# Performance work log

Hardware: AMD Instinct MI355X
Metric: run time of the kernel (lower is better)

## Reference

```python
import jax, jax.numpy as jnp
import numpy as np

HEAD_NUM = 8
QKV_DIM = 16
SQRT_EMBEDDING_DIM = 11.313708498984761  # sqrt(128)
LOGIT_CLIPPING = 10.0


def _reshape_by_heads(x):
    # x: [B, n, H*D] -> [B, H, n, D]
    B, n, _ = x.shape
    return x.reshape(B, n, HEAD_NUM, QKV_DIM).transpose(0, 2, 1, 3)


def setup_inputs() -> dict:
    key = jax.random.key(0)
    ks = jax.random.split(key, 12)
    B, P, N, E = 64, 500, 501, 128
    HD = HEAD_NUM * QKV_DIM
    s = 0.05
    return {
        "encoded_last_node": jax.random.normal(ks[0], (B, P, E), jnp.float32),
        "load": jax.random.uniform(ks[1], (B, P), jnp.float32),
        "ninf_mask": jnp.zeros((B, P, N), jnp.float32),
        "encoded_nodes": jax.random.normal(ks[2], (B, N, E), jnp.float32),
        "Wq_last": jax.random.normal(ks[3], (E + 1, HD), jnp.float32) * s,
        "Wk": jax.random.normal(ks[4], (E, HD), jnp.float32) * s,
        "Wv": jax.random.normal(ks[5], (E, HD), jnp.float32) * s,
        "mhc_W": jax.random.normal(ks[6], (HD, E), jnp.float32) * s,
        "mhc_b": jax.random.normal(ks[7], (E,), jnp.float32) * s,
        "new": jax.random.normal(ks[8], (B, HD, HD), jnp.float32) * s,
        "new_bias": jax.random.normal(ks[9], (B, 1, HD), jnp.float32) * s,
        "new_2": jax.random.normal(ks[10], (B, HD, HD), jnp.float32) * s,
        "new_bias_2": jax.random.normal(ks[11], (B, 1, HD), jnp.float32) * s,
    }


def reference(encoded_last_node, load, ninf_mask, encoded_nodes,
              Wq_last, Wk, Wv, mhc_W, mhc_b,
              new, new_bias, new_2, new_bias_2):
    B, P, E = encoded_last_node.shape
    # set_kv
    k = _reshape_by_heads(encoded_nodes @ Wk)            # [B,H,N,D]
    v = _reshape_by_heads(encoded_nodes @ Wv)            # [B,H,N,D]
    single_head_key = encoded_nodes.transpose(0, 2, 1)   # [B,E,N]

    # q from (last node embedding, load)
    input_cat = jnp.concatenate([encoded_last_node, load[:, :, None]], axis=2)  # [B,P,E+1]
    q = _reshape_by_heads(input_cat @ Wq_last)           # [B,H,P,D]

    # multi-head attention
    score = jnp.einsum('bhpd,bhnd->bhpn', q, k) / jnp.sqrt(jnp.float32(QKV_DIM))
    score = score + ninf_mask[:, None, :, :]
    attn = jax.nn.softmax(score, axis=3)
    out = jnp.einsum('bhpn,bhnd->bhpd', attn, v)         # [B,H,P,D]
    out_concat = out.transpose(0, 2, 1, 3).reshape(B, P, HEAD_NUM * QKV_DIM)

    # per-batch affine + relu + residual
    residual = out_concat
    h = jax.nn.relu(jnp.matmul(out_concat, new) + new_bias)
    h = jnp.matmul(h, new_2) + new_bias_2 + residual

    mh_atten_out = h @ mhc_W + mhc_b                     # [B,P,E]

    score2 = jnp.matmul(mh_atten_out, single_head_key)   # [B,P,N]
    score_clipped = LOGIT_CLIPPING * jnp.tanh(score2 / SQRT_EMBEDDING_DIM)
    probs = jax.nn.softmax(score_clipped + ninf_mask, axis=2)
    return probs
```

## Files before the change

kernel.cpp:

```cpp
#include <hip/hip_runtime.h>
#include <hip/hip_bf16.h>
#include <math.h>

typedef float f4 __attribute__((ext_vector_type(4)));

#define BATCH 64
#define PP 500
#define NN 501

__global__ __launch_bounds__(256) void k_proj_q(
    const float* __restrict__ Xn,
    const float* __restrict__ Ld,
    const float* __restrict__ Wq,
    float* __restrict__ Q)
{
  __shared__ float xs[64*132];
  const int t = threadIdx.x;
  const int r0 = blockIdx.x * 64;
  for (int i = t; i < 64*32; i += 256) {
    int r = i >> 5, k4 = (i & 31) << 2;
    *(f4*)(xs + r*132 + k4) = *(const f4*)(Xn + (size_t)(r0+r)*128 + k4);
  }
  if (t < 64) xs[t*132 + 128] = Ld[r0 + t];
  __syncthreads();
  const int tr = t >> 5, tc = t & 31;
  float acc[8][4];
  #pragma unroll
  for (int i = 0; i < 8; i++)
    #pragma unroll
    for (int c = 0; c < 4; c++) acc[i][c] = 0.f;
  for (int k4 = 0; k4 < 128; k4 += 4) {
    f4 x[8], w[4];
    #pragma unroll
    for (int j = 0; j < 4; j++) w[j] = *(const f4*)(Wq + (size_t)(k4+j)*128 + tc*4);
    #pragma unroll
    for (int i = 0; i < 8; i++) x[i] = *(const f4*)(xs + (tr*8+i)*132 + k4);
    #pragma unroll
    for (int i = 0; i < 8; i++)
      #pragma unroll
      for (int j = 0; j < 4; j++)
        #pragma unroll
        for (int c = 0; c < 4; c++)
          acc[i][c] += x[i][j] * w[j][c];
  }
  {
    f4 w = *(const f4*)(Wq + (size_t)128*128 + tc*4);
    #pragma unroll
    for (int i = 0; i < 8; i++) {
      float xv = xs[(tr*8+i)*132 + 128];
      #pragma unroll
      for (int c = 0; c < 4; c++) acc[i][c] += xv * w[c];
    }
  }
  #pragma unroll
  for (int i = 0; i < 8; i++) {
    f4 o;
    #pragma unroll
    for (int c = 0; c < 4; c++) o[c] = acc[i][c];
    *(f4*)(Q + (size_t)(r0 + tr*8 + i)*128 + tc*4) = o;
  }
}

__global__ __launch_bounds__(256) void k_proj_kv(
    const float* __restrict__ Xn,
    const float* __restrict__ Wk, const float* __restrict__ Wv,
    float* __restrict__ K_, float* __restrict__ V_)
{
  __shared__ float xs[64*132];
  const int t = threadIdx.x;
  const int r0 = blockIdx.x * 64;
  for (int i = t; i < 64*32; i += 256) {
    int r = i >> 5, k4 = (i & 31) << 2;
    *(f4*)(xs + r*132 + k4) = *(const f4*)(Xn + (size_t)(r0+r)*128 + k4);
  }
  __syncthreads();
  const int tr = t >> 5, tc = t & 31;
  float accK[8][4], accV[8][4];
  #pragma unroll
  for (int i = 0; i < 8; i++)
    #pragma unroll
    for (int c = 0; c < 4; c++) { accK[i][c] = 0.f; accV[i][c] = 0.f; }
  for (int k4 = 0; k4 < 128; k4 += 4) {
    f4 x[8], wk[4], wv[4];
    #pragma unroll
    for (int j = 0; j < 4; j++) {
      wk[j] = *(const f4*)(Wk + (size_t)(k4+j)*128 + tc*4);
      wv[j] = *(const f4*)(Wv + (size_t)(k4+j)*128 + tc*4);
    }
    #pragma unroll
    for (int i = 0; i < 8; i++) x[i] = *(const f4*)(xs + (tr*8+i)*132 + k4);
    #pragma unroll
    for (int i = 0; i < 8; i++)
      #pragma unroll
      for (int j = 0; j < 4; j++)
        #pragma unroll
        for (int c = 0; c < 4; c++) {
          accK[i][c] += x[i][j] * wk[j][c];
          accV[i][c] += x[i][j] * wv[j][c];
        }
  }
  #pragma unroll
  for (int i = 0; i < 8; i++) {
    f4 ok, ov;
    #pragma unroll
    for (int c = 0; c < 4; c++) { ok[c] = accK[i][c]; ov[c] = accV[i][c]; }
    *(f4*)(K_ + (size_t)(r0 + tr*8 + i)*128 + tc*4) = ok;
    *(f4*)(V_ + (size_t)(r0 + tr*8 + i)*128 + tc*4) = ov;
  }
}

__global__ __launch_bounds__(256, 3) void k_attn(
    const float* __restrict__ Q, const float* __restrict__ K_, const float* __restrict__ V_,
    const float* __restrict__ Msk, float* __restrict__ OC)
{
  __shared__ float ks[32*132];
  __shared__ float vs[32*132];
  __shared__ float mks[32*33];
  const int blk = blockIdx.x;
  const int b  = blk >> 4;
  const int pt = blk & 15;
  const int p0 = pt * 32;
  const int t = threadIdx.x;
  const int h   = t >> 5;
  const int row = t & 31;
  const bool pvalid = (p0 + row) < PP;
  const int p = pvalid ? (p0 + row) : (PP - 1);

  f4 q0, q1, q2, q3;
  {
    const float* qrow = Q + ((size_t)b*PP + p)*128 + h*16;
    q0 = *(const f4*)(qrow);
    q1 = *(const f4*)(qrow + 4);
    q2 = *(const f4*)(qrow + 8);
    q3 = *(const f4*)(qrow + 12);
  }
  const float* mgrow = Msk + ((size_t)b*PP + p)*NN;

  float m_r = -1e30f, l_r = 0.f;
  f4 o0 = {0.f,0.f,0.f,0.f}, o1 = o0, o2 = o0, o3 = o0;

  for (int c0 = 0; c0 < NN; c0 += 32) {
    __syncthreads();
    #pragma unroll
    for (int u = 0; u < 4; u++) {
      int i = t + u*256;
      int n = i >> 5, d4 = (i & 31) << 2;
      int ng = c0 + n;
      f4 kv = {0.f,0.f,0.f,0.f}, vv = {0.f,0.f,0.f,0.f};
      if (ng < NN) {
        kv = *(const f4*)(K_ + ((size_t)b*NN + ng)*128 + d4);
        vv = *(const f4*)(V_ + ((size_t)b*NN + ng)*128 + d4);
      }
      *(f4*)(ks + n*132 + d4) = kv;
      *(f4*)(vs + n*132 + d4) = vv;
    }
    {
      int mr = t >> 3, nq = (t & 7) << 2;
      int grow = p0 + mr; if (grow >= PP) grow = PP - 1;
      const float* gm = Msk + ((size_t)b*PP + grow)*NN + c0;
      float* dm = mks + mr*33 + nq;
      #pragma unroll
      for (int j = 0; j < 4; j++)
        dm[j] = (c0 + nq + j < NN) ? gm[nq + j] : -1e30f;
    }
    __syncthreads();

    const float* ksh = ks + h*16;
    const float* vsh = vs + h*16;
    const float* mrw = mks + row*33;
    #pragma unroll
    for (int n = 0; n < 32; n++) {
      const float* kf = ksh + n*132;
      f4 k0 = *(const f4*)(kf);
      f4 k1 = *(const f4*)(kf + 4);
      f4 k2 = *(const f4*)(kf + 8);
      f4 k3 = *(const f4*)(kf + 12);
      float s = 0.f;
      #pragma unroll
      for (int d = 0; d < 4; d++) s += q0[d]*k0[d];
      #pragma unroll
      for (int d = 0; d < 4; d++) s += q1[d]*k1[d];
      #pragma unroll
      for (int d = 0; d < 4; d++) s += q2[d]*k2[d];
      #pragma unroll
      for (int d = 0; d < 4; d++) s += q3[d]*k3[d];
      s = s*0.25f + mrw[n];
      if (s > m_r) {
        float cc = __expf(m_r - s);
        m_r = s;
        l_r *= cc;
        o0 *= cc; o1 *= cc; o2 *= cc; o3 *= cc;
      }
      float e = __expf(s - m_r);
      l_r += e;
      const float* vf = vsh + n*132;
      o0 += e * *(const f4*)(vf);
      o1 += e * *(const f4*)(vf + 4);
      o2 += e * *(const f4*)(vf + 8);
      o3 += e * *(const f4*)(vf + 12);
    }
  }

  if (pvalid) {
    float inv = 1.f / l_r;
    float* orow = OC + ((size_t)b*PP + p)*128 + h*16;
    *(f4*)(orow)      = o0 * inv;
    *(f4*)(orow + 4)  = o1 * inv;
    *(f4*)(orow + 8)  = o2 * inv;
    *(f4*)(orow + 12) = o3 * inv;
  }
}

__global__ __launch_bounds__(256) void k_ffn(
    const float* __restrict__ OC, const float* __restrict__ Wn, const float* __restrict__ Bn,
    const float* __restrict__ Wn2, const float* __restrict__ Bn2,
    const float* __restrict__ Wm, const float* __restrict__ Bm,
    float* __restrict__ MH)
{
  __shared__ float xs[64*132];
  __shared__ float hs[64*132];
  const int blk = blockIdx.x; const int b = blk >> 3, rb = blk & 7;
  const int r0 = rb*64;
  const int nv = min(64, PP - r0);
  const int t = threadIdx.x;
  const int tr = t >> 5, tc = t & 31;
  const float* ocb = OC + (size_t)b*PP*128;
  for (int i = t; i < 64*32; i += 256) {
    int r = i >> 5, k4 = (i & 31) << 2;
    f4 v = {0.f,0.f,0.f,0.f};
    if (r < nv) v = *(const f4*)(ocb + (size_t)(r0+r)*128 + k4);
    *(f4*)(xs + r*132 + k4) = v;
  }
  __syncthreads();
  {
    const float* W1 = Wn + (size_t)b*16384;
    float acc[8][4];
    #pragma unroll
    for (int i = 0; i < 8; i++)
      #pragma unroll
      for (int c = 0; c < 4; c++) acc[i][c] = 0.f;
    for (int k4 = 0; k4 < 128; k4 += 4) {
      f4 x[8], w[4];
      #pragma unroll
      for (int j = 0; j < 4; j++) w[j] = *(const f4*)(W1 + (size_t)(k4+j)*128 + tc*4);
      #pragma unroll
      for (int i = 0; i < 8; i++) x[i] = *(const f4*)(xs + (tr*8+i)*132 + k4);
      #pragma unroll
      for (int i = 0; i < 8; i++)
        #pragma unroll
        for (int j = 0; j < 4; j++)
          #pragma unroll
          for (int c = 0; c < 4; c++)
            acc[i][c] += x[i][j] * w[j][c];
    }
    f4 b1 = *(const f4*)(Bn + b*128 + tc*4);
    #pragma unroll
    for (int i = 0; i < 8; i++) {
      f4 o;
      #pragma unroll
      for (int c = 0; c < 4; c++) o[c] = fmaxf(acc[i][c] + b1[c], 0.f);
      *(f4*)(hs + (tr*8+i)*132 + tc*4) = o;
    }
  }
  __syncthreads();
  float h2[8][4];
  {
    const float* W2 = Wn2 + (size_t)b*16384;
    float acc[8][4];
    #pragma unroll
    for (int i = 0; i < 8; i++)
      #pragma unroll
      for (int c = 0; c < 4; c++) acc[i][c] = 0.f;
    for (int k4 = 0; k4 < 128; k4 += 4) {
      f4 x[8], w[4];
      #pragma unroll
      for (int j = 0; j < 4; j++) w[j] = *(const f4*)(W2 + (size_t)(k4+j)*128 + tc*4);
      #pragma unroll
      for (int i = 0; i < 8; i++) x[i] = *(const f4*)(hs + (tr*8+i)*132 + k4);
      #pragma unroll
      for (int i = 0; i < 8; i++)
        #pragma unroll
        for (int j = 0; j < 4; j++)
          #pragma unroll
          for (int c = 0; c < 4; c++)
            acc[i][c] += x[i][j] * w[j][c];
    }
    f4 b2 = *(const f4*)(Bn2 + b*128 + tc*4);
    #pragma unroll
    for (int i = 0; i < 8; i++)
      #pragma unroll
      for (int c = 0; c < 4; c++)
        h2[i][c] = acc[i][c] + b2[c] + xs[(tr*8+i)*132 + tc*4 + c];
  }
  __syncthreads();
  #pragma unroll
  for (int i = 0; i < 8; i++) {
    f4 o;
    #pragma unroll
    for (int c = 0; c < 4; c++) o[c] = h2[i][c];
    *(f4*)(hs + (tr*8+i)*132 + tc*4) = o;
  }
  __syncthreads();
  {
    float acc[8][4];
    #pragma unroll
    for (int i = 0; i < 8; i++)
      #pragma unroll
      for (int c = 0; c < 4; c++) acc[i][c] = 0.f;
    for (int k4 = 0; k4 < 128; k4 += 4) {
      f4 x[8], w[4];
      #pragma unroll
      for (int j = 0; j < 4; j++) w[j] = *(const f4*)(Wm + (size_t)(k4+j)*128 + tc*4);
      #pragma unroll
      for (int i = 0; i < 8; i++) x[i] = *(const f4*)(hs + (tr*8+i)*132 + k4);
      #pragma unroll
      for (int i = 0; i < 8; i++)
        #pragma unroll
        for (int j = 0; j < 4; j++)
          #pragma unroll
          for (int c = 0; c < 4; c++)
            acc[i][c] += x[i][j] * w[j][c];
    }
    f4 b3 = *(const f4*)(Bm + tc*4);
    #pragma unroll
    for (int i = 0; i < 8; i++) {
      if (tr*8 + i < nv) {
        f4 o;
        #pragma unroll
        for (int c = 0; c < 4; c++) o[c] = acc[i][c] + b3[c];
        *(f4*)(MH + ((size_t)b*PP + r0 + tr*8 + i)*128 + tc*4) = o;
      }
    }
  }
}

__global__ __launch_bounds__(256, 3) void k_final(
    const float* __restrict__ MH, const float* __restrict__ EN,
    const float* __restrict__ Msk, float* __restrict__ OUT)
{
  __shared__ float ms[32*132];
  __shared__ float es[64*132];
  const int blk = blockIdx.x; const int b = blk >> 4, rb = blk & 15;
  const int r0 = rb*32; const int nv = min(32, PP - r0);
  const int t = threadIdx.x;
  const int tr = t >> 5, tc = t & 31;
  const float* mhb = MH + (size_t)(b*PP + r0)*128;
  for (int i = t; i < 32*32; i += 256) {
    int r = i >> 5, k4 = (i & 31) << 2;
    f4 v = {0.f,0.f,0.f,0.f};
    if (r < nv) v = *(const f4*)(mhb + (size_t)r*128 + k4);
    *(f4*)(ms + r*132 + k4) = v;
  }
  const float* enb = EN + (size_t)b*NN*128;
  float s[8][4][2];
  #pragma unroll
  for (int nt = 0; nt < 8; nt++) {
    const int n0 = nt*64;
    __syncthreads();
    for (int i = t; i < 64*32; i += 256) {
      int n = i >> 5, k4 = (i & 31) << 2;
      f4 v = {0.f,0.f,0.f,0.f};
      if (n0 + n < NN) v = *(const f4*)(enb + (size_t)(n0+n)*128 + k4);
      *(f4*)(es + n*132 + k4) = v;
    }
    __syncthreads();
    float acc[4][2];
    #pragma unroll
    for (int i = 0; i < 4; i++) { acc[i][0] = 0.f; acc[i][1] = 0.f; }
    #pragma unroll 8
    for (int k4 = 0; k4 < 128; k4 += 4) {
      f4 x[4];
      #pragma unroll
      for (int i = 0; i < 4; i++) x[i] = *(const f4*)(ms + (tr*4+i)*132 + k4);
      f4 e0 = *(const f4*)(es + tc*132 + k4);
      f4 e1 = *(const f4*)(es + (tc+32)*132 + k4);
      #pragma unroll
      for (int i = 0; i < 4; i++)
        #pragma unroll
        for (int j = 0; j < 4; j++) {
          acc[i][0] += x[i][j]*e0[j];
          acc[i][1] += x[i][j]*e1[j];
        }
    }
    #pragma unroll
    for (int i = 0; i < 4; i++) {
      s[nt][i][0] = acc[i][0];
      s[nt][i][1] = acc[i][1];
    }
  }
  const float* mkb = Msk + (size_t)(b*PP + r0)*NN;
  #pragma unroll
  for (int nt = 0; nt < 8; nt++)
    #pragma unroll
    for (int i = 0; i < 4; i++)
      #pragma unroll
      for (int c = 0; c < 2; c++) {
        int r = tr*4 + i, n = nt*64 + tc + c*32;
        float val = -INFINITY;
        if (r < nv && n < NN) {
          float E = __expf(s[nt][i][c] * 0.17677669529663687f);
          val = 10.f - 20.f/(E + 1.f) + mkb[(size_t)r*NN + n];
        }
        s[nt][i][c] = val;
      }
  float* ob = OUT + (size_t)(b*PP + r0)*NN;
  #pragma unroll
  for (int i = 0; i < 4; i++) {
    float m = -INFINITY;
    #pragma unroll
    for (int nt = 0; nt < 8; nt++)
      #pragma unroll
      for (int c = 0; c < 2; c++) m = fmaxf(m, s[nt][i][c]);
    #pragma unroll
    for (int o = 16; o > 0; o >>= 1) m = fmaxf(m, __shfl_xor(m, o, 32));
    float l = 0.f;
    #pragma unroll
    for (int nt = 0; nt < 8; nt++)
      #pragma unroll
      for (int c = 0; c < 2; c++) {
        float e_ = __expf(s[nt][i][c] - m);
        s[nt][i][c] = e_;
        l += e_;
      }
    #pragma unroll
    for (int o = 16; o > 0; o >>= 1) l += __shfl_xor(l, o, 32);
    const int r = tr*4 + i;
    if (r < nv) {
      float inv = 1.f / l;
      float* orow = ob + (size_t)r*NN;
      #pragma unroll
      for (int nt = 0; nt < 8; nt++)
        #pragma unroll
        for (int c = 0; c < 2; c++) {
          int n = nt*64 + tc + c*32;
          if (n < NN) orow[n] = s[nt][i][c] * inv;
        }
    }
  }
}

extern "C" void kernel_launch(void* const* d_in, const int* in_sizes, int n_in,
                              void* d_out, int out_size, void* d_ws, size_t ws_size,
                              hipStream_t stream) {
  const float* eln  = (const float*)d_in[0];
  const float* load = (const float*)d_in[1];
  const float* mask = (const float*)d_in[2];
  const float* en   = (const float*)d_in[3];
  const float* Wq   = (const float*)d_in[4];
  const float* Wk   = (const float*)d_in[5];
  const float* Wv   = (const float*)d_in[6];
  const float* Wm   = (const float*)d_in[7];
  const float* Bm   = (const float*)d_in[8];
  const float* Wn   = (const float*)d_in[9];
  const float* Bn   = (const float*)d_in[10];
  const float* Wn2  = (const float*)d_in[11];
  const float* Bn2  = (const float*)d_in[12];
  float* out = (float*)d_out;
  float* ws  = (float*)d_ws;
  float* Q   = ws;
  float* K_  = ws + 4096000;
  float* V_  = ws + 8200192;
  float* OC  = ws + 12304384;
  float* MH  = ws + 16400384;
  hipLaunchKernelGGL(k_proj_q,  dim3(500),  dim3(256), 0, stream, eln, load, Wq, Q);
  hipLaunchKernelGGL(k_proj_kv, dim3(501),  dim3(256), 0, stream, en, Wk, Wv, K_, V_);
  hipLaunchKernelGGL(k_attn,    dim3(1024), dim3(256), 0, stream, Q, K_, V_, mask, OC);
  hipLaunchKernelGGL(k_ffn,     dim3(512),  dim3(256), 0, stream, OC, Wn, Bn, Wn2, Bn2, Wm, Bm, MH);
  hipLaunchKernelGGL(k_final,   dim3(1024), dim3(256), 0, stream, MH, en, mask, out);
}
```

Baseline: 443.5 us.

## Merge Q/KV projections into one launch and double attention rows per thread

```diff
diff --git a/kernel.cpp b/kernel.cpp
--- a/kernel.cpp
+++ b/kernel.cpp
@@ -8,104 +8,99 @@
 #define PP 500
 #define NN 501
 
-__global__ __launch_bounds__(256) void k_proj_q(
+__global__ __launch_bounds__(256) void k_proj(
+    const float* __restrict__ Xq,
+    const float* __restrict__ Ld,
     const float* __restrict__ Xn,
-    const float* __restrict__ Ld,
     const float* __restrict__ Wq,
-    float* __restrict__ Q)
+    const float* __restrict__ Wk, const float* __restrict__ Wv,
+    float* __restrict__ Q, float* __restrict__ K_, float* __restrict__ V_)
 {
   __shared__ float xs[64*132];
   const int t = threadIdx.x;
-  const int r0 = blockIdx.x * 64;
-  for (int i = t; i < 64*32; i += 256) {
-    int r = i >> 5, k4 = (i & 31) << 2;
-    *(f4*)(xs + r*132 + k4) = *(const f4*)(Xn + (size_t)(r0+r)*128 + k4);
-  }
-  if (t < 64) xs[t*132 + 128] = Ld[r0 + t];
-  __syncthreads();
   const int tr = t >> 5, tc = t & 31;
-  float acc[8][4];
-  #pragma unroll
-  for (int i = 0; i < 8; i++)
-    #pragma unroll
-    for (int c = 0; c < 4; c++) acc[i][c] = 0.f;
-  for (int k4 = 0; k4 < 128; k4 += 4) {
-    f4 x[8], w[4];
-    #pragma unroll
-    for (int j = 0; j < 4; j++) w[j] = *(const f4*)(Wq + (size_t)(k4+j)*128 + tc*4);
-    #pragma unroll
-    for (int i = 0; i < 8; i++) x[i] = *(const f4*)(xs + (tr*8+i)*132 + k4);
-    #pragma unroll
-    for (int i = 0; i < 8; i++)
-      #pragma unroll
-      for (int j = 0; j < 4; j++)
-        #pragma unroll
-        for (int c = 0; c < 4; c++)
-          acc[i][c] += x[i][j] * w[j][c];
-  }
-  {
-    f4 w = *(const f4*)(Wq + (size_t)128*128 + tc*4);
+  if (blockIdx.x < 500) {
+    const int r0 = blockIdx.x * 64;
+    for (int i = t; i < 64*32; i += 256) {
+      int r = i >> 5, k4 = (i & 31) << 2;
+      *(f4*)(xs + r*132 + k4) = *(const f4*)(Xq + (size_t)(r0+r)*128 + k4);
+    }
+    if (t < 64) xs[t*132 + 128] = Ld[r0 + t];
+    __syncthreads();
+    float acc[8][4];
+    #pragma unroll
+    for (int i = 0; i < 8; i++)
+      #pragma unroll
+      for (int c = 0; c < 4; c++) acc[i][c] = 0.f;
+    for (int k4 = 0; k4 < 128; k4 += 4) {
+      f4 x[8], w[4];
+      #pragma unroll
+      for (int j = 0; j < 4; j++) w[j] = *(const f4*)(Wq + (size_t)(k4+j)*128 + tc*4);
+      #pragma unroll
+      for (int i = 0; i < 8; i++) x[i] = *(const f4*)(xs + (tr*8+i)*132 + k4);
+      #pragma unroll
+      for (int i = 0; i < 8; i++)
+        #pragma unroll
+        for (int j = 0; j < 4; j++)
+          #pragma unroll
+          for (int c = 0; c < 4; c++)
+            acc[i][c] += x[i][j] * w[j][c];
+    }
+    {
+      f4 w = *(const f4*)(Wq + (size_t)128*128 + tc*4);
+      #pragma unroll
+      for (int i = 0; i < 8; i++) {
+        float xv = xs[(tr*8+i)*132 + 128];
+        #pragma unroll
+        for (int c = 0; c < 4; c++) acc[i][c] += xv * w[c];
+      }
+    }
     #pragma unroll
     for (int i = 0; i < 8; i++) {
-      float xv = xs[(tr*8+i)*132 + 128];
-      #pragma unroll
-      for (int c = 0; c < 4; c++) acc[i][c] += xv * w[c];
-    }
-  }
-  #pragma unroll
-  for (int i = 0; i < 8; i++) {
-    f4 o;
-    #pragma unroll
-    for (int c = 0; c < 4; c++) o[c] = acc[i][c];
-    *(f4*)(Q + (size_t)(r0 + tr*8 + i)*128 + tc*4) = o;
-  }
-}
-
-__global__ __launch_bounds__(256) void k_proj_kv(
-    const float* __restrict__ Xn,
-    const float* __restrict__ Wk, const float* __restrict__ Wv,
-    float* __restrict__ K_, float* __restrict__ V_)
-{
-  __shared__ float xs[64*132];
-  const int t = threadIdx.x;
-  const int r0 = blockIdx.x * 64;
-  for (int i = t; i < 64*32; i += 256) {
-    int r = i >> 5, k4 = (i & 31) << 2;
-    *(f4*)(xs + r*132 + k4) = *(const f4*)(Xn + (size_t)(r0+r)*128 + k4);
-  }
-  __syncthreads();
-  const int tr = t >> 5, tc = t & 31;
-  float accK[8][4], accV[8][4];
-  #pragma unroll
-  for (int i = 0; i < 8; i++)
-    #pragma unroll
-    for (int c = 0; c < 4; c++) { accK[i][c] = 0.f; accV[i][c] = 0.f; }
-  for (int k4 = 0; k4 < 128; k4 += 4) {
-    f4 x[8], wk[4], wv[4];
-    #pragma unroll
-    for (int j = 0; j < 4; j++) {
-      wk[j] = *(const f4*)(Wk + (size_t)(k4+j)*128 + tc*4);
-      wv[j] = *(const f4*)(Wv + (size_t)(k4+j)*128 + tc*4);
-    }
-    #pragma unroll
-    for (int i = 0; i < 8; i++) x[i] = *(const f4*)(xs + (tr*8+i)*132 + k4);
-    #pragma unroll
-    for (int i = 0; i < 8; i++)
-      #pragma unroll
-      for (int j = 0; j < 4; j++)
-        #pragma unroll
-        for (int c = 0; c < 4; c++) {
-          accK[i][c] += x[i][j] * wk[j][c];
-          accV[i][c] += x[i][j] * wv[j][c];
-        }
-  }
-  #pragma unroll
-  for (int i = 0; i < 8; i++) {
-    f4 ok, ov;
-    #pragma unroll
-    for (int c = 0; c < 4; c++) { ok[c] = accK[i][c]; ov[c] = accV[i][c]; }
-    *(f4*)(K_ + (size_t)(r0 + tr*8 + i)*128 + tc*4) = ok;
-    *(f4*)(V_ + (size_t)(r0 + tr*8 + i)*128 + tc*4) = ov;
+      f4 o;
+      #pragma unroll
+      for (int c = 0; c < 4; c++) o[c] = acc[i][c];
+      *(f4*)(Q + (size_t)(r0 + tr*8 + i)*128 + tc*4) = o;
+    }
+  } else {
+    const int r0 = (blockIdx.x - 500) * 64;
+    for (int i = t; i < 64*32; i += 256) {
+      int r = i >> 5, k4 = (i & 31) << 2;
+      *(f4*)(xs + r*132 + k4) = *(const f4*)(Xn + (size_t)(r0+r)*128 + k4);
+    }
+    __syncthreads();
+    float accK[8][4], accV[8][4];
+    #pragma unroll
+    for (int i = 0; i < 8; i++)
+      #pragma unroll
+      for (int c = 0; c < 4; c++) { accK[i][c] = 0.f; accV[i][c] = 0.f; }
+    for (int k4 = 0; k4 < 128; k4 += 4) {
+      f4 x[8], wk[4], wv[4];
+      #pragma unroll
+      for (int j = 0; j < 4; j++) {
+        wk[j] = *(const f4*)(Wk + (size_t)(k4+j)*128 + tc*4);
+        wv[j] = *(const f4*)(Wv + (size_t)(k4+j)*128 + tc*4);
+      }
+      #pragma unroll
+      for (int i = 0; i < 8; i++) x[i] = *(const f4*)(xs + (tr*8+i)*132 + k4);
+      #pragma unroll
+      for (int i = 0; i < 8; i++)
+        #pragma unroll
+        for (int j = 0; j < 4; j++)
+          #pragma unroll
+          for (int c = 0; c < 4; c++) {
+            accK[i][c] += x[i][j] * wk[j][c];
+            accV[i][c] += x[i][j] * wv[j][c];
+          }
+    }
+    #pragma unroll
+    for (int i = 0; i < 8; i++) {
+      f4 ok, ov;
+      #pragma unroll
+      for (int c = 0; c < 4; c++) { ok[c] = accK[i][c]; ov[c] = accV[i][c]; }
+      *(f4*)(K_ + (size_t)(r0 + tr*8 + i)*128 + tc*4) = ok;
+      *(f4*)(V_ + (size_t)(r0 + tr*8 + i)*128 + tc*4) = ov;
+    }
   }
 }
 
@@ -113,31 +108,38 @@
     const float* __restrict__ Q, const float* __restrict__ K_, const float* __restrict__ V_,
     const float* __restrict__ Msk, float* __restrict__ OC)
 {
-  __shared__ float ks[32*132];
-  __shared__ float vs[32*132];
-  __shared__ float mks[32*33];
+  __shared__ float ks[32*128];
+  __shared__ float vs[32*128];
+  __shared__ float mkt[32*64];
   const int blk = blockIdx.x;
-  const int b  = blk >> 4;
-  const int pt = blk & 15;
-  const int p0 = pt * 32;
+  const int b  = blk >> 3;
+  const int pt = blk & 7;
+  const int p0 = pt * 64;
   const int t = threadIdx.x;
-  const int h   = t >> 5;
-  const int row = t & 31;
-  const bool pvalid = (p0 + row) < PP;
-  const int p = pvalid ? (p0 + row) : (PP - 1);
-
-  f4 q0, q1, q2, q3;
+  const int h    = t >> 5;
+  const int rowA = t & 31;
+  const int rowB = rowA + 32;
+  const int pA = p0 + rowA;
+  const int pB0 = p0 + rowB;
+  const bool bvalid = pB0 < PP;
+  const int pB = bvalid ? pB0 : (PP - 1);
+
+  f4 qA0, qA1, qA2, qA3, qB0, qB1, qB2, qB3;
   {
-    const float* qrow = Q + ((size_t)b*PP + p)*128 + h*16;
-    q0 = *(const f4*)(qrow);
-    q1 = *(const f4*)(qrow + 4);
-    q2 = *(const f4*)(qrow + 8);
-    q3 = *(const f4*)(qrow + 12);
-  }
-  const float* mgrow = Msk + ((size_t)b*PP + p)*NN;
-
-  float m_r = -1e30f, l_r = 0.f;
-  f4 o0 = {0.f,0.f,0.f,0.f}, o1 = o0, o2 = o0, o3 = o0;
+    const float* qa = Q + ((size_t)b*PP + pA)*128 + h*16;
+    qA0 = *(const f4*)(qa); qA1 = *(const f4*)(qa+4); qA2 = *(const f4*)(qa+8); qA3 = *(const f4*)(qa+12);
+    const float* qb = Q + ((size_t)b*PP + pB)*128 + h*16;
+    qB0 = *(const f4*)(qb); qB1 = *(const f4*)(qb+4); qB2 = *(const f4*)(qb+8); qB3 = *(const f4*)(qb+12);
+  }
+
+  float mA = -1e30f, lA = 0.f, mB = -1e30f, lB = 0.f;
+  f4 oA0 = {0.f,0.f,0.f,0.f}, oA1 = oA0, oA2 = oA0, oA3 = oA0;
+  f4 oB0 = oA0, oB1 = oA0, oB2 = oA0, oB3 = oA0;
+
+  const int mr = t >> 3;
+  const int nq = (t & 7) << 2;
+  const float* gmA = Msk + ((size_t)b*PP + p0 + mr)*NN;
+  const float* gmB = Msk + ((size_t)b*PP + min(p0 + mr + 32, PP-1))*NN;
 
   for (int c0 = 0; c0 < NN; c0 += 32) {
     __syncthreads();
@@ -151,63 +153,72 @@
         kv = *(const f4*)(K_ + ((size_t)b*NN + ng)*128 + d4);
         vv = *(const f4*)(V_ + ((size_t)b*NN + ng)*128 + d4);
       }
-      *(f4*)(ks + n*132 + d4) = kv;
-      *(f4*)(vs + n*132 + d4) = vv;
-    }
-    {
-      int mr = t >> 3, nq = (t & 7) << 2;
-      int grow = p0 + mr; if (grow >= PP) grow = PP - 1;
-      const float* gm = Msk + ((size_t)b*PP + grow)*NN + c0;
-      float* dm = mks + mr*33 + nq;
-      #pragma unroll
-      for (int j = 0; j < 4; j++)
-        dm[j] = (c0 + nq + j < NN) ? gm[nq + j] : -1e30f;
-    }
-    __syncthreads();
-
-    const float* ksh = ks + h*16;
-    const float* vsh = vs + h*16;
-    const float* mrw = mks + row*33;
+      *(f4*)(ks + n*128 + d4) = kv;
+      *(f4*)(vs + n*128 + d4) = vv;
+    }
+    #pragma unroll
+    for (int j = 0; j < 4; j++) {
+      int nn = c0 + nq + j;
+      bool cv = nn < NN;
+      float a  = cv ? gmA[nn] : -1e30f;
+      float bb = cv ? gmB[nn] : -1e30f;
+      mkt[(nq+j)*64 + mr]      = a;
+      mkt[(nq+j)*64 + mr + 32] = bb;
+    }
+    __syncthreads();
+
     #pragma unroll
     for (int n = 0; n < 32; n++) {
-      const float* kf = ksh + n*132;
+      const float* kf = ks + n*128 + h*16;
       f4 k0 = *(const f4*)(kf);
       f4 k1 = *(const f4*)(kf + 4);
       f4 k2 = *(const f4*)(kf + 8);
       f4 k3 = *(const f4*)(kf + 12);
-      float s = 0.f;
-      #pragma unroll
-      for (int d = 0; d < 4; d++) s += q0[d]*k0[d];
-      #pragma unroll
-      for (int d = 0; d < 4; d++) s += q1[d]*k1[d];
-      #pragma unroll
-      for (int d = 0; d < 4; d++) s += q2[d]*k2[d];
-      #pragma unroll
-      for (int d = 0; d < 4; d++) s += q3[d]*k3[d];
-      s = s*0.25f + mrw[n];
-      if (s > m_r) {
-        float cc = __expf(m_r - s);
-        m_r = s;
-        l_r *= cc;
-        o0 *= cc; o1 *= cc; o2 *= cc; o3 *= cc;
-      }
-      float e = __expf(s - m_r);
-      l_r += e;
-      const float* vf = vsh + n*132;
-      o0 += e * *(const f4*)(vf);
-      o1 += e * *(const f4*)(vf + 4);
-      o2 += e * *(const f4*)(vf + 8);
-      o3 += e * *(const f4*)(vf + 12);
-    }
-  }
-
-  if (pvalid) {
-    float inv = 1.f / l_r;
-    float* orow = OC + ((size_t)b*PP + p)*128 + h*16;
-    *(f4*)(orow)      = o0 * inv;
-    *(f4*)(orow + 4)  = o1 * inv;
-    *(f4*)(orow + 8)  = o2 * inv;
-    *(f4*)(orow + 12) = o3 * inv;
+      float sA = 0.f, sB = 0.f;
+      #pragma unroll
+      for (int d = 0; d < 4; d++) {
+        sA += qA0[d]*k0[d]; sB += qB0[d]*k0[d];
+        sA += qA1[d]*k1[d]; sB += qB1[d]*k1[d];
+        sA += qA2[d]*k2[d]; sB += qB2[d]*k2[d];
+        sA += qA3[d]*k3[d]; sB += qB3[d]*k3[d];
+      }
+      sA = sA*0.25f + mkt[n*64 + rowA];
+      sB = sB*0.25f + mkt[n*64 + rowB];
+      if (sA > mA) {
+        float cc = __expf(mA - sA); mA = sA; lA *= cc;
+        oA0 *= cc; oA1 *= cc; oA2 *= cc; oA3 *= cc;
+      }
+      if (sB > mB) {
+        float cc = __expf(mB - sB); mB = sB; lB *= cc;
+        oB0 *= cc; oB1 *= cc; oB2 *= cc; oB3 *= cc;
+      }
+      float eA = __expf(sA - mA); lA += eA;
+      float eB = __expf(sB - mB); lB += eB;
+      const float* vf = vs + n*128 + h*16;
+      f4 v0 = *(const f4*)(vf);
+      f4 v1 = *(const f4*)(vf + 4);
+      f4 v2 = *(const f4*)(vf + 8);
+      f4 v3 = *(const f4*)(vf + 12);
+      oA0 += eA*v0; oA1 += eA*v1; oA2 += eA*v2; oA3 += eA*v3;
+      oB0 += eB*v0; oB1 += eB*v1; oB2 += eB*v2; oB3 += eB*v3;
+    }
+  }
+
+  {
+    float inv = 1.f / lA;
+    float* orow = OC + ((size_t)b*PP + pA)*128 + h*16;
+    *(f4*)(orow)      = oA0 * inv;
+    *(f4*)(orow + 4)  = oA1 * inv;
+    *(f4*)(orow + 8)  = oA2 * inv;
+    *(f4*)(orow + 12) = oA3 * inv;
+  }
+  if (bvalid) {
+    float inv = 1.f / lB;
+    float* orow = OC + ((size_t)b*PP + pB)*128 + h*16;
+    *(f4*)(orow)      = oB0 * inv;
+    *(f4*)(orow + 4)  = oB1 * inv;
+    *(f4*)(orow + 8)  = oB2 * inv;
+    *(f4*)(orow + 12) = oB3 * inv;
   }
 }
 
@@ -462,9 +473,8 @@
   float* V_  = ws + 8200192;
   float* OC  = ws + 12304384;
   float* MH  = ws + 16400384;
-  hipLaunchKernelGGL(k_proj_q,  dim3(500),  dim3(256), 0, stream, eln, load, Wq, Q);
-  hipLaunchKernelGGL(k_proj_kv, dim3(501),  dim3(256), 0, stream, en, Wk, Wv, K_, V_);
-  hipLaunchKernelGGL(k_attn,    dim3(1024), dim3(256), 0, stream, Q, K_, V_, mask, OC);
-  hipLaunchKernelGGL(k_ffn,     dim3(512),  dim3(256), 0, stream, OC, Wn, Bn, Wn2, Bn2, Wm, Bm, MH);
-  hipLaunchKernelGGL(k_final,   dim3(1024), dim3(256), 0, stream, MH, en, mask, out);
+  hipLaunchKernelGGL(k_proj,  dim3(1001), dim3(256), 0, stream, eln, load, en, Wq, Wk, Wv, Q, K_, V_);
+  hipLaunchKernelGGL(k_attn,  dim3(512),  dim3(256), 0, stream, Q, K_, V_, mask, OC);
+  hipLaunchKernelGGL(k_ffn,   dim3(512),  dim3(256), 0, stream, OC, Wn, Bn, Wn2, Bn2, Wm, Bm, MH);
+  hipLaunchKernelGGL(k_final, dim3(1024), dim3(256), 0, stream, MH, en, mask, out);
 }
```

After: 472.0 us. 6.4% more time.

## Merge projection kernels and register-prefetch next K/V/mask tile in attention

Applied to the files above, without the earlier changes.

```diff
diff --git a/kernel.cpp b/kernel.cpp
--- a/kernel.cpp
+++ b/kernel.cpp
@@ -8,108 +8,103 @@
 #define PP 500
 #define NN 501
 
-__global__ __launch_bounds__(256) void k_proj_q(
+__global__ __launch_bounds__(256) void k_proj(
+    const float* __restrict__ Xq,
+    const float* __restrict__ Ld,
     const float* __restrict__ Xn,
-    const float* __restrict__ Ld,
     const float* __restrict__ Wq,
-    float* __restrict__ Q)
+    const float* __restrict__ Wk, const float* __restrict__ Wv,
+    float* __restrict__ Q, float* __restrict__ K_, float* __restrict__ V_)
 {
   __shared__ float xs[64*132];
   const int t = threadIdx.x;
-  const int r0 = blockIdx.x * 64;
-  for (int i = t; i < 64*32; i += 256) {
-    int r = i >> 5, k4 = (i & 31) << 2;
-    *(f4*)(xs + r*132 + k4) = *(const f4*)(Xn + (size_t)(r0+r)*128 + k4);
-  }
-  if (t < 64) xs[t*132 + 128] = Ld[r0 + t];
-  __syncthreads();
   const int tr = t >> 5, tc = t & 31;
-  float acc[8][4];
-  #pragma unroll
-  for (int i = 0; i < 8; i++)
-    #pragma unroll
-    for (int c = 0; c < 4; c++) acc[i][c] = 0.f;
-  for (int k4 = 0; k4 < 128; k4 += 4) {
-    f4 x[8], w[4];
-    #pragma unroll
-    for (int j = 0; j < 4; j++) w[j] = *(const f4*)(Wq + (size_t)(k4+j)*128 + tc*4);
-    #pragma unroll
-    for (int i = 0; i < 8; i++) x[i] = *(const f4*)(xs + (tr*8+i)*132 + k4);
-    #pragma unroll
-    for (int i = 0; i < 8; i++)
-      #pragma unroll
-      for (int j = 0; j < 4; j++)
-        #pragma unroll
-        for (int c = 0; c < 4; c++)
-          acc[i][c] += x[i][j] * w[j][c];
-  }
-  {
-    f4 w = *(const f4*)(Wq + (size_t)128*128 + tc*4);
+  if (blockIdx.x < 500) {
+    const int r0 = blockIdx.x * 64;
+    for (int i = t; i < 64*32; i += 256) {
+      int r = i >> 5, k4 = (i & 31) << 2;
+      *(f4*)(xs + r*132 + k4) = *(const f4*)(Xq + (size_t)(r0+r)*128 + k4);
+    }
+    if (t < 64) xs[t*132 + 128] = Ld[r0 + t];
+    __syncthreads();
+    float acc[8][4];
+    #pragma unroll
+    for (int i = 0; i < 8; i++)
+      #pragma unroll
+      for (int c = 0; c < 4; c++) acc[i][c] = 0.f;
+    for (int k4 = 0; k4 < 128; k4 += 4) {
+      f4 x[8], w[4];
+      #pragma unroll
+      for (int j = 0; j < 4; j++) w[j] = *(const f4*)(Wq + (size_t)(k4+j)*128 + tc*4);
+      #pragma unroll
+      for (int i = 0; i < 8; i++) x[i] = *(const f4*)(xs + (tr*8+i)*132 + k4);
+      #pragma unroll
+      for (int i = 0; i < 8; i++)
+        #pragma unroll
+        for (int j = 0; j < 4; j++)
+          #pragma unroll
+          for (int c = 0; c < 4; c++)
+            acc[i][c] += x[i][j] * w[j][c];
+    }
+    {
+      f4 w = *(const f4*)(Wq + (size_t)128*128 + tc*4);
+      #pragma unroll
+      for (int i = 0; i < 8; i++) {
+        float xv = xs[(tr*8+i)*132 + 128];
+        #pragma unroll
+        for (int c = 0; c < 4; c++) acc[i][c] += xv * w[c];
+      }
+    }
     #pragma unroll
     for (int i = 0; i < 8; i++) {
-      float xv = xs[(tr*8+i)*132 + 128];
-      #pragma unroll
-      for (int c = 0; c < 4; c++) acc[i][c] += xv * w[c];
-    }
-  }
-  #pragma unroll
-  for (int i = 0; i < 8; i++) {
-    f4 o;
-    #pragma unroll
-    for (int c = 0; c < 4; c++) o[c] = acc[i][c];
-    *(f4*)(Q + (size_t)(r0 + tr*8 + i)*128 + tc*4) = o;
+      f4 o;
+      #pragma unroll
+      for (int c = 0; c < 4; c++) o[c] = acc[i][c];
+      *(f4*)(Q + (size_t)(r0 + tr*8 + i)*128 + tc*4) = o;
+    }
+  } else {
+    const int r0 = (blockIdx.x - 500) * 64;
+    for (int i = t; i < 64*32; i += 256) {
+      int r = i >> 5, k4 = (i & 31) << 2;
+      *(f4*)(xs + r*132 + k4) = *(const f4*)(Xn + (size_t)(r0+r)*128 + k4);
+    }
+    __syncthreads();
+    float accK[8][4], accV[8][4];
+    #pragma unroll
+    for (int i = 0; i < 8; i++)
+      #pragma unroll
+      for (int c = 0; c < 4; c++) { accK[i][c] = 0.f; accV[i][c] = 0.f; }
+    for (int k4 = 0; k4 < 128; k4 += 4) {
+      f4 x[8], wk[4], wv[4];
+      #pragma unroll
+      for (int j = 0; j < 4; j++) {
+        wk[j] = *(const f4*)(Wk + (size_t)(k4+j)*128 + tc*4);
+        wv[j] = *(const f4*)(Wv + (size_t)(k4+j)*128 + tc*4);
+      }
+      #pragma unroll
+      for (int i = 0; i < 8; i++) x[i] = *(const f4*)(xs + (tr*8+i)*132 + k4);
+      #pragma unroll
+      for (int i = 0; i < 8; i++)
+        #pragma unroll
+        for (int j = 0; j < 4; j++)
+          #pragma unroll
+          for (int c = 0; c < 4; c++) {
+            accK[i][c] += x[i][j] * wk[j][c];
+            accV[i][c] += x[i][j] * wv[j][c];
+          }
+    }
+    #pragma unroll
+    for (int i = 0; i < 8; i++) {
+      f4 ok, ov;
+      #pragma unroll
+      for (int c = 0; c < 4; c++) { ok[c] = accK[i][c]; ov[c] = accV[i][c]; }
+      *(f4*)(K_ + (size_t)(r0 + tr*8 + i)*128 + tc*4) = ok;
+      *(f4*)(V_ + (size_t)(r0 + tr*8 + i)*128 + tc*4) = ov;
+    }
   }
 }
 
-__global__ __launch_bounds__(256) void k_proj_kv(
-    const float* __restrict__ Xn,
-    const float* __restrict__ Wk, const float* __restrict__ Wv,
-    float* __restrict__ K_, float* __restrict__ V_)
-{
-  __shared__ float xs[64*132];
-  const int t = threadIdx.x;
-  const int r0 = blockIdx.x * 64;
-  for (int i = t; i < 64*32; i += 256) {
-    int r = i >> 5, k4 = (i & 31) << 2;
-    *(f4*)(xs + r*132 + k4) = *(const f4*)(Xn + (size_t)(r0+r)*128 + k4);
-  }
-  __syncthreads();
-  const int tr = t >> 5, tc = t & 31;
-  float accK[8][4], accV[8][4];
-  #pragma unroll
-  for (int i = 0; i < 8; i++)
-    #pragma unroll
-    for (int c = 0; c < 4; c++) { accK[i][c] = 0.f; accV[i][c] = 0.f; }
-  for (int k4 = 0; k4 < 128; k4 += 4) {
-    f4 x[8], wk[4], wv[4];
-    #pragma unroll
-    for (int j = 0; j < 4; j++) {
-      wk[j] = *(const f4*)(Wk + (size_t)(k4+j)*128 + tc*4);
-      wv[j] = *(const f4*)(Wv + (size_t)(k4+j)*128 + tc*4);
-    }
-    #pragma unroll
-    for (int i = 0; i < 8; i++) x[i] = *(const f4*)(xs + (tr*8+i)*132 + k4);
-    #pragma unroll
-    for (int i = 0; i < 8; i++)
-      #pragma unroll
-      for (int j = 0; j < 4; j++)
-        #pragma unroll
-        for (int c = 0; c < 4; c++) {
-          accK[i][c] += x[i][j] * wk[j][c];
-          accV[i][c] += x[i][j] * wv[j][c];
-        }
-  }
-  #pragma unroll
-  for (int i = 0; i < 8; i++) {
-    f4 ok, ov;
-    #pragma unroll
-    for (int c = 0; c < 4; c++) { ok[c] = accK[i][c]; ov[c] = accV[i][c]; }
-    *(f4*)(K_ + (size_t)(r0 + tr*8 + i)*128 + tc*4) = ok;
-    *(f4*)(V_ + (size_t)(r0 + tr*8 + i)*128 + tc*4) = ov;
-  }
-}
-
-__global__ __launch_bounds__(256, 3) void k_attn(
+__global__ __launch_bounds__(256, 4) void k_attn(
     const float* __restrict__ Q, const float* __restrict__ K_, const float* __restrict__ V_,
     const float* __restrict__ Msk, float* __restrict__ OC)
 {
@@ -134,36 +129,65 @@
     q2 = *(const f4*)(qrow + 8);
     q3 = *(const f4*)(qrow + 12);
   }
-  const float* mgrow = Msk + ((size_t)b*PP + p)*NN;
+
+  const int sn  = t >> 3;
+  const int mr = t >> 3, nq = (t & 7) << 2;
+  const int grow = min(p0 + mr, PP - 1);
+  const float* gm = Msk + ((size_t)b*PP + grow)*NN;
 
   float m_r = -1e30f, l_r = 0.f;
   f4 o0 = {0.f,0.f,0.f,0.f}, o1 = o0, o2 = o0, o3 = o0;
 
+  f4 kp[2], vp[2]; float mk[4];
+  {
+    int i0 = t, i1 = t + 256;
+    int n0r = i0 >> 3, d40 = (i0 & 7) << 4;
+  }
+  f4 kpre[4], vpre[4];
+  #pragma unroll
+  for (int u = 0; u < 4; u++) {
+    int i = t + u*256;
+    int n = i >> 5, d4 = (i & 31) << 2;
+    kpre[u] = *(const f4*)(K_ + ((size_t)b*NN + n)*128 + d4);
+    vpre[u] = *(const f4*)(V_ + ((size_t)b*NN + n)*128 + d4);
+  }
+  #pragma unroll
+  for (int j = 0; j < 4; j++)
+    mk[j] = (nq + j < NN) ? gm[nq + j] : -1e30f;
+
   for (int c0 = 0; c0 < NN; c0 += 32) {
-    __syncthreads();
     #pragma unroll
     for (int u = 0; u < 4; u++) {
       int i = t + u*256;
       int n = i >> 5, d4 = (i & 31) << 2;
-      int ng = c0 + n;
-      f4 kv = {0.f,0.f,0.f,0.f}, vv = {0.f,0.f,0.f,0.f};
-      if (ng < NN) {
-        kv = *(const f4*)(K_ + ((size_t)b*NN + ng)*128 + d4);
-        vv = *(const f4*)(V_ + ((size_t)b*NN + ng)*128 + d4);
-      }
-      *(f4*)(ks + n*132 + d4) = kv;
-      *(f4*)(vs + n*132 + d4) = vv;
+      *(f4*)(ks + n*132 + d4) = kpre[u];
+      *(f4*)(vs + n*132 + d4) = vpre[u];
     }
     {
-      int mr = t >> 3, nq = (t & 7) << 2;
-      int grow = p0 + mr; if (grow >= PP) grow = PP - 1;
-      const float* gm = Msk + ((size_t)b*PP + grow)*NN + c0;
       float* dm = mks + mr*33 + nq;
       #pragma unroll
+      for (int j = 0; j < 4; j++) dm[j] = mk[j];
+    }
+    __syncthreads();
+
+    const int c1 = c0 + 32;
+    if (c1 < NN) {
+      #pragma unroll
+      for (int u = 0; u < 4; u++) {
+        int i = t + u*256;
+        int n = i >> 5, d4 = (i & 31) << 2;
+        int ng = c1 + n;
+        f4 kv = {0.f,0.f,0.f,0.f}, vv = {0.f,0.f,0.f,0.f};
+        if (ng < NN) {
+          kv = *(const f4*)(K_ + ((size_t)b*NN + ng)*128 + d4);
+          vv = *(const f4*)(V_ + ((size_t)b*NN + ng)*128 + d4);
+        }
+        kpre[u] = kv; vpre[u] = vv;
+      }
+      #pragma unroll
       for (int j = 0; j < 4; j++)
-        dm[j] = (c0 + nq + j < NN) ? gm[nq + j] : -1e30f;
-    }
-    __syncthreads();
+        mk[j] = (c1 + nq + j < NN) ? gm[c1 + nq + j] : -1e30f;
+    }
 
     const float* ksh = ks + h*16;
     const float* vsh = vs + h*16;
@@ -199,6 +223,7 @@
       o2 += e * *(const f4*)(vf + 8);
       o3 += e * *(const f4*)(vf + 12);
     }
+    __syncthreads();
   }
 
   if (pvalid) {
@@ -462,9 +487,8 @@
   float* V_  = ws + 8200192;
   float* OC  = ws + 12304384;
   float* MH  = ws + 16400384;
-  hipLaunchKernelGGL(k_proj_q,  dim3(500),  dim3(256), 0, stream, eln, load, Wq, Q);
-  hipLaunchKernelGGL(k_proj_kv, dim3(501),  dim3(256), 0, stream, en, Wk, Wv, K_, V_);
-  hipLaunchKernelGGL(k_attn,    dim3(1024), dim3(256), 0, stream, Q, K_, V_, mask, OC);
-  hipLaunchKernelGGL(k_ffn,     dim3(512),  dim3(256), 0, stream, OC, Wn, Bn, Wn2, Bn2, Wm, Bm, MH);
-  hipLaunchKernelGGL(k_final,   dim3(1024), dim3(256), 0, stream, MH, en, mask, out);
+  hipLaunchKernelGGL(k_proj,  dim3(1001), dim3(256), 0, stream, eln, load, en, Wq, Wk, Wv, Q, K_, V_);
+  hipLaunchKernelGGL(k_attn,  dim3(1024), dim3(256), 0, stream, Q, K_, V_, mask, OC);
+  hipLaunchKernelGGL(k_ffn,   dim3(512),  dim3(256), 0, stream, OC, Wn, Bn, Wn2, Bn2, Wm, Bm, MH);
+  hipLaunchKernelGGL(k_final, dim3(1024), dim3(256), 0, stream, MH, en, mask, out);
 }
```

After: 436.9 us. About the same (-1.5%).
